# Kernel optimization log

Hardware: AMD Instinct MI355X
Metric: run time of the kernel (lower is better)

Reference implementation:

```python
import jax, jax.numpy as jnp
import numpy as np

NTOKEN = 100000
INPUT_DIM = 2000
OUTPUT_DIM = 8
B, L = 64, 200


def setup_inputs() -> dict:
    key = jax.random.key(0)
    k1, k2, k3 = jax.random.split(key, 3)
    inp = jax.random.randint(k1, (B, L), 0, NTOKEN)                  # user ids
    user_repost_matrix = jax.random.uniform(k2, (NTOKEN, INPUT_DIM), dtype=jnp.float32)
    W = jax.random.normal(k3, (OUTPUT_DIM, INPUT_DIM), dtype=jnp.float32) * (2.0 / (INPUT_DIM + OUTPUT_DIM)) ** 0.5
    b = jnp.zeros((OUTPUT_DIM,), dtype=jnp.float32)
    return {"input": inp, "user_repost_matrix": user_repost_matrix, "W": W, "b": b}


def reference(input, user_repost_matrix, W, b):
    # one-hot(input) @ user_repost_matrix == row gather of user_repost_matrix
    B_, L_ = input.shape
    rows = jnp.take(user_repost_matrix, input.reshape(-1), axis=0)   # [B*L, input_dim]
    out = rows @ W.T + b                                             # [B*L, output_dim]
    return out.reshape(B_, L_, -1)                                   # [B, L, 8]
```

## Files before the change

kernel.cpp:

```cpp
#include <hip/hip_runtime.h>


#define IN_DIM   2000
#define IN_DIM4  500
#define PAD_DIM4 512
#define OUT_DIM  8

__global__ __launch_bounds__(256, 2)
void item_encoder_kernel(const int* __restrict__ ids,
                         const float* __restrict__ U,
                         const float* __restrict__ W,
                         const float* __restrict__ bias,
                         float* __restrict__ out,
                         int T)
{
    __shared__ float4 wlds[OUT_DIM * PAD_DIM4];

    const int tid = threadIdx.x;

    const float4* Wv = (const float4*)W;
    #pragma unroll
    for (int i = 0; i < 16; ++i) {
        int d  = tid + i * 256;
        int j  = d >> 9;
        int k4 = d & 511;
        float4 v = make_float4(0.f, 0.f, 0.f, 0.f);
        if (k4 < IN_DIM4) v = Wv[j * IN_DIM4 + k4];
        wlds[d] = v;
    }
    __syncthreads();

    const int lane    = tid & 63;
    const int wave    = tid >> 6;
    const int wave_id = blockIdx.x * 4 + wave;
    const int nwaves  = gridDim.x * 4;

    for (int t = wave_id; t < T; t += nwaves) {
        const int id = ids[t];
        const float4* row = (const float4*)(U + (size_t)id * IN_DIM);

        float4 x[8];
        #pragma unroll
        for (int i = 0; i < 8; ++i) {
            const int k4 = lane + i * 64;
            x[i] = (k4 < IN_DIM4) ? row[k4] : make_float4(0.f, 0.f, 0.f, 0.f);
        }

        float acc[OUT_DIM];
        #pragma unroll
        for (int j = 0; j < OUT_DIM; ++j) acc[j] = 0.f;

        #pragma unroll
        for (int i = 0; i < 8; ++i) {
            const int k4 = lane + i * 64;
            const float4 xv = x[i];
            #pragma unroll
            for (int j = 0; j < OUT_DIM; ++j) {
                const float4 w = wlds[j * PAD_DIM4 + k4];
                acc[j] += xv.x * w.x + xv.y * w.y + xv.z * w.z + xv.w * w.w;
            }
        }

        #pragma unroll
        for (int off = 32; off > 0; off >>= 1) {
            #pragma unroll
            for (int j = 0; j < OUT_DIM; ++j)
                acc[j] += __shfl_xor(acc[j], off, 64);
        }

        if (lane < OUT_DIM)
            out[(size_t)t * OUT_DIM + lane] = acc[lane] + bias[lane];
    }
}

extern "C" void kernel_launch(void* const* d_in, const int* in_sizes, int n_in,
                              void* d_out, int out_size, void* d_ws, size_t ws_size,
                              hipStream_t stream)
{
    const int*   ids  = (const int*)d_in[0];
    const float* U    = (const float*)d_in[1];
    const float* W    = (const float*)d_in[2];
    const float* bias = (const float*)d_in[3];
    float*       out  = (float*)d_out;

    const int T = in_sizes[0];

    item_encoder_kernel<<<dim3(512), dim3(256), 0, stream>>>(ids, U, W, bias, out, T);
}
```

Measured before the change: 920.2 us.

## Process two rows per wave and use transpose-style butterfly reduction

Each wave now gathers two token rows per iteration, so it issues twice as many loads in flight and reuses every LDS weight read for both rows. The 8-output cross-lane reduction becomes a recursive halving butterfly in which each step exchanges half of the remaining outputs, which cuts the shuffle count. Lanes 0-7 end up holding the outputs in a permuted order, which jmap maps back when writing. The cost is higher register pressure (16 float4 row registers plus 16 accumulators), which could lower occupancy under the 256,2 launch bounds.

```diff
diff --git a/kernel.cpp b/kernel.cpp
--- a/kernel.cpp
+++ b/kernel.cpp
@@ -35,41 +35,84 @@
     const int wave_id = blockIdx.x * 4 + wave;
     const int nwaves  = gridDim.x * 4;
 
-    for (int t = wave_id; t < T; t += nwaves) {
-        const int id = ids[t];
-        const float4* row = (const float4*)(U + (size_t)id * IN_DIM);
+    const int jmap = ((lane & 1) << 2) | (lane & 2) | ((lane >> 2) & 1);
+    const float bj = bias[jmap];
 
-        float4 x[8];
+    for (int t0 = wave_id; t0 < T; t0 += 2 * nwaves) {
+        const int t1   = t0 + nwaves;
+        const bool has1 = (t1 < T);
+
+        const int id0 = ids[t0];
+        const int id1 = has1 ? ids[t1] : id0;
+        const float4* r0 = (const float4*)(U + (size_t)id0 * IN_DIM);
+        const float4* r1 = (const float4*)(U + (size_t)id1 * IN_DIM);
+
+        float4 x0[8], x1[8];
         #pragma unroll
         for (int i = 0; i < 8; ++i) {
-            const int k4 = lane + i * 64;
-            x[i] = (k4 < IN_DIM4) ? row[k4] : make_float4(0.f, 0.f, 0.f, 0.f);
+            const int  k4 = lane + i * 64;
+            const bool in = (k4 < IN_DIM4);
+            x0[i] = in ? r0[k4] : make_float4(0.f, 0.f, 0.f, 0.f);
+            x1[i] = in ? r1[k4] : make_float4(0.f, 0.f, 0.f, 0.f);
         }
 
-        float acc[OUT_DIM];
+        float acc0[OUT_DIM], acc1[OUT_DIM];
         #pragma unroll
-        for (int j = 0; j < OUT_DIM; ++j) acc[j] = 0.f;
+        for (int j = 0; j < OUT_DIM; ++j) { acc0[j] = 0.f; acc1[j] = 0.f; }
 
         #pragma unroll
         for (int i = 0; i < 8; ++i) {
             const int k4 = lane + i * 64;
-            const float4 xv = x[i];
+            const float4 a = x0[i];
+            const float4 c = x1[i];
             #pragma unroll
             for (int j = 0; j < OUT_DIM; ++j) {
                 const float4 w = wlds[j * PAD_DIM4 + k4];
-                acc[j] += xv.x * w.x + xv.y * w.y + xv.z * w.z + xv.w * w.w;
+                acc0[j] += a.x * w.x + a.y * w.y + a.z * w.z + a.w * w.w;
+                acc1[j] += c.x * w.x + c.y * w.y + c.z * w.z + c.w * w.w;
             }
         }
 
-        #pragma unroll
-        for (int off = 32; off > 0; off >>= 1) {
+        float v0, v1;
+        {
+            float a4[4], c4[4];
             #pragma unroll
-            for (int j = 0; j < OUT_DIM; ++j)
-                acc[j] += __shfl_xor(acc[j], off, 64);
+            for (int m = 0; m < 4; ++m) {
+                float sa = (lane & 1) ? acc0[m] : acc0[m + 4];
+                float ka = (lane & 1) ? acc0[m + 4] : acc0[m];
+                a4[m] = ka + __shfl_xor(sa, 1, 64);
+                float sc = (lane & 1) ? acc1[m] : acc1[m + 4];
+                float kc = (lane & 1) ? acc1[m + 4] : acc1[m];
+                c4[m] = kc + __shfl_xor(sc, 1, 64);
+            }
+            float a2[2], c2[2];
+            #pragma unroll
+            for (int m = 0; m < 2; ++m) {
+                float sa = (lane & 2) ? a4[m] : a4[m + 2];
+                float ka = (lane & 2) ? a4[m + 2] : a4[m];
+                a2[m] = ka + __shfl_xor(sa, 2, 64);
+                float sc = (lane & 2) ? c4[m] : c4[m + 2];
+                float kc = (lane & 2) ? c4[m + 2] : c4[m];
+                c2[m] = kc + __shfl_xor(sc, 2, 64);
+            }
+            {
+                float sa = (lane & 4) ? a2[0] : a2[1];
+                float ka = (lane & 4) ? a2[1] : a2[0];
+                v0 = ka + __shfl_xor(sa, 4, 64);
+                float sc = (lane & 4) ? c2[0] : c2[1];
+                float kc = (lane & 4) ? c2[1] : c2[0];
+                v1 = kc + __shfl_xor(sc, 4, 64);
+            }
+            v0 += __shfl_xor(v0, 8, 64);  v1 += __shfl_xor(v1, 8, 64);
+            v0 += __shfl_xor(v0, 16, 64); v1 += __shfl_xor(v1, 16, 64);
+            v0 += __shfl_xor(v0, 32, 64); v1 += __shfl_xor(v1, 32, 64);
         }
 
-        if (lane < OUT_DIM)
-            out[(size_t)t * OUT_DIM + lane] = acc[lane] + bias[lane];
+        if (lane < OUT_DIM) {
+            out[(size_t)t0 * OUT_DIM + jmap] = v0 + bj;
+            if (has1)
+                out[(size_t)t1 * OUT_DIM + jmap] = v1 + bj;
+        }
     }
 }
 
```

Result: no change. 913.4 us (-0.7%).
